# Optimization experiments

Hardware: AMD Instinct MI355X
Metric: run time of the kernel (lower is better)

The kernel has to match this reference:

```python
import jax, jax.numpy as jnp
import numpy as np

MEAN = 0.0
SIGMA = 2.0


def setup_inputs() -> dict:
    key = jax.random.key(0)
    B, S, D = 8, 1024, 1024
    ks = jax.random.split(key, 7)
    scale = 1.0 / np.sqrt(D)
    return {
        "x": jax.random.normal(ks[0], (B, S, D), dtype=jnp.float32),
        "Wa": jax.random.normal(ks[1], (D, D), dtype=jnp.float32) * scale,
        "ba": jnp.zeros((D,), dtype=jnp.float32),
        "Wshift": jax.random.normal(ks[2], (D, D), dtype=jnp.float32) * scale,
        "bshift": jnp.zeros((D,), dtype=jnp.float32),
        "Wscale": jax.random.normal(ks[3], (D, D), dtype=jnp.float32) * scale,
        "bscale": jnp.zeros((D,), dtype=jnp.float32),
    }


def _gaussian_matrix(S, dtype):
    # Row t holds the flipped, normalized Gaussian kernel of length t+1:
    # weight on position j (j<=t) is exp(-((t-j)-mean)^2/(2*sigma^2)), row-normalized.
    idx = jnp.arange(S)
    d = idx[:, None] - idx[None, :]  # t - j
    g = jnp.exp(-((d.astype(dtype) - MEAN) ** 2) / (2.0 * SIGMA ** 2))
    g = jnp.where(d >= 0, g, 0.0)  # causal (growing window)
    return g / jnp.sum(g, axis=1, keepdims=True)


def reference(x, Wa, ba, Wshift, bshift, Wscale, bscale):
    S = x.shape[1]
    W = _gaussian_matrix(S, x.dtype)  # [S, S] lower-triangular
    filtered = jnp.einsum("tj,bjd->btd", W, x)  # causal Gaussian-weighted sum
    shift = filtered @ Wshift + bshift
    scale = filtered @ Wscale + bscale
    affine = jax.nn.relu(x @ Wa + ba)
    return scale * affine + shift
```

## Files before the change

### kernel.cpp

```cpp
#include <hip/hip_runtime.h>
#include <stdint.h>

typedef __attribute__((ext_vector_type(8))) __bf16 bf16x8;
typedef __attribute__((ext_vector_type(4))) float f32x4;

__device__ __forceinline__ unsigned short f2bf(float f) {
  union { float f; unsigned int u; } v; v.f = f;
  unsigned int u = v.u;
  u = (u + 0x7FFFu + ((u >> 16) & 1u)) >> 16;
  return (unsigned short)u;
}
__device__ __forceinline__ float bf2f(unsigned int u) {
  union { unsigned int u; float f; } v; v.u = u << 16;
  return v.f;
}

__global__ __launch_bounds__(256) void xconv(
    const float* __restrict__ x, unsigned short* __restrict__ xb)
{
  const size_t i = ((size_t)blockIdx.x * 256 + threadIdx.x) * 8;
  const float4 a = *(const float4*)(x + i);
  const float4 b = *(const float4*)(x + i + 4);
  ushort4 o0, o1;
  o0.x = f2bf(a.x); o0.y = f2bf(a.y); o0.z = f2bf(a.z); o0.w = f2bf(a.w);
  o1.x = f2bf(b.x); o1.y = f2bf(b.y); o1.z = f2bf(b.z); o1.w = f2bf(b.w);
  *(ushort4*)(xb + i) = o0;
  *(ushort4*)(xb + i + 4) = o1;
}

__global__ __launch_bounds__(256) void wconv(
    const float* __restrict__ Wa, const float* __restrict__ Wsh,
    const float* __restrict__ Wsc, unsigned short* __restrict__ Wt3)
{
  const float* W;
  if (blockIdx.z == 0)      W = Wa;
  else if (blockIdx.z == 1) W = Wsh;
  else                      W = Wsc;
  unsigned short* O = Wt3 + (size_t)blockIdx.z * 1024 * 1024;
  const int k0 = blockIdx.x * 64;
  const int n0 = blockIdx.y * 64;
  __shared__ float t[64][65];
  const int r = threadIdx.x >> 4;
  const int c4 = threadIdx.x & 15;
#pragma unroll
  for (int i = 0; i < 4; ++i) {
    const int row = r + i * 16;
    const float4 v = *(const float4*)(W + (size_t)(k0 + row) * 1024 + n0 + c4 * 4);
    t[row][c4 * 4 + 0] = v.x; t[row][c4 * 4 + 1] = v.y;
    t[row][c4 * 4 + 2] = v.z; t[row][c4 * 4 + 3] = v.w;
  }
  __syncthreads();
#pragma unroll
  for (int i = 0; i < 4; ++i) {
    const int nr = r + i * 16;
    ushort4 o;
    o.x = f2bf(t[c4 * 4 + 0][nr]);
    o.y = f2bf(t[c4 * 4 + 1][nr]);
    o.z = f2bf(t[c4 * 4 + 2][nr]);
    o.w = f2bf(t[c4 * 4 + 3][nr]);
    *(ushort4*)(O + (size_t)(n0 + nr) * 1024 + k0 + c4 * 4) = o;
  }
}

__global__ __launch_bounds__(256, 2) void gemm_all(
    const unsigned short* __restrict__ xb, const unsigned short* __restrict__ Wt3,
    const float* __restrict__ ba, const float* __restrict__ bsh,
    const float* __restrict__ bsc, float* __restrict__ out)
{
  __shared__ __attribute__((aligned(16))) char lds[54016];
  unsigned short* sX = (unsigned short*)lds;
  unsigned short* sB = (unsigned short*)(lds + 20480);
  unsigned short* ysh_l = (unsigned short*)lds;
  unsigned short* ysc_l = (unsigned short*)(lds + 18688);
  unsigned short* aff_l = (unsigned short*)(lds + 37376);

  const int tid = threadIdx.x;
  const int lane = tid & 63;
  const int wid = tid >> 6;
  const int wm = wid >> 1;
  const int wn = wid & 1;
  const int lr = lane & 15;
  const int lk = lane >> 4;

  const int bid = blockIdx.x;
  const int xcd = bid & 7;
  const int rr_ = bid >> 3;
  const int ntl = rr_ & 15;
  const int mg  = rr_ >> 4;
  const int bm0 = (xcd + (mg << 3)) * 128;
  const int bn0 = ntl * 64;
  const bool first = (xcd == 0);

  f32x4 acc[3][4][2];
  f32x4 hacc[2][2];
  const f32x4 z = {0.f, 0.f, 0.f, 0.f};
#pragma unroll
  for (int a = 0; a < 3; ++a)
#pragma unroll
    for (int m = 0; m < 4; ++m)
#pragma unroll
      for (int j = 0; j < 2; ++j) acc[a][m][j] = z;
#pragma unroll
  for (int a = 0; a < 2; ++a)
#pragma unroll
    for (int j = 0; j < 2; ++j) hacc[a][j] = z;

  auto stage = [&](int k0) {
#pragma unroll
    for (int p = 0; p < 5; ++p) {
      const int po = (p * 256 + tid) * 16;
      const int row = po >> 7;
      const int lo = po ^ ((row & 7) << 4);
      const int colu = (lo & 127) >> 1;
      int rel = row - 16;
      if (rel < 0 && first) rel = 0;
      if (rel > 127) rel = 0;
      const unsigned short* src = xb + (size_t)(bm0 + rel) * 1024 + k0 + colu;
      __builtin_amdgcn_global_load_lds(
          (const __attribute__((address_space(1))) void*)src,
          (__attribute__((address_space(3))) void*)(sX + (p * 256 + (wid << 6)) * 8),
          16, 0, 0);
    }
#pragma unroll
    for (int mat = 0; mat < 3; ++mat)
#pragma unroll
      for (int p = 0; p < 2; ++p) {
        const int po = (p * 256 + tid) * 16;
        const int row = po >> 7;
        const int lo = po ^ ((row & 7) << 4);
        const int colu = (lo & 127) >> 1;
        const unsigned short* src =
            Wt3 + ((size_t)mat << 20) + (size_t)(bn0 + row) * 1024 + k0 + colu;
        __builtin_amdgcn_global_load_lds(
            (const __attribute__((address_space(1))) void*)src,
            (__attribute__((address_space(3))) void*)(sB + mat * 4096 + (p * 256 + (wid << 6)) * 8),
            16, 0, 0);
      }
  };
  auto rd = [&](const unsigned short* base, int row, int s) -> bf16x8 {
    const int po = row * 128 + (((s * 32 + lk * 8) * 2) ^ ((row & 7) << 4));
    return *(const bf16x8*)((const char*)base + po);
  };

  stage(0);

  for (int kt = 0; kt < 16; ++kt) {
    __syncthreads();

#pragma unroll
    for (int s = 0; s < 2; ++s) {
      bf16x8 ax[4], bb[3][2], hax;
#pragma unroll
      for (int m = 0; m < 4; ++m)
        ax[m] = rd(sX, 16 + wm * 64 + m * 16 + lr, s);
#pragma unroll
      for (int mat = 0; mat < 3; ++mat)
#pragma unroll
        for (int jj = 0; jj < 2; ++jj)
          bb[mat][jj] = rd(sB + mat * 4096, wn * 32 + jj * 16 + lr, s);
      if (wm == 0) hax = rd(sX, lr, s);

      __builtin_amdgcn_s_setprio(1);
#pragma unroll
      for (int m = 0; m < 4; ++m)
#pragma unroll
        for (int mat = 0; mat < 3; ++mat)
#pragma unroll
          for (int jj = 0; jj < 2; ++jj)
            acc[mat][m][jj] = __builtin_amdgcn_mfma_f32_16x16x32_bf16(
                ax[m], bb[mat][jj], acc[mat][m][jj], 0, 0, 0);
      if (wm == 0) {
#pragma unroll
        for (int mat = 1; mat < 3; ++mat)
#pragma unroll
          for (int jj = 0; jj < 2; ++jj)
            hacc[mat - 1][jj] = __builtin_amdgcn_mfma_f32_16x16x32_bf16(
                hax, bb[mat][jj], hacc[mat - 1][jj], 0, 0, 0);
      }
      __builtin_amdgcn_s_setprio(0);
    }

    __syncthreads();
    if (kt + 1 < 16) stage((kt + 1) * 64);
  }

#pragma unroll
  for (int jj = 0; jj < 2; ++jj) {
    const int nn = wn * 32 + jj * 16 + lr;
    const float Ba = ba[bn0 + nn];
#pragma unroll
    for (int m = 0; m < 4; ++m)
#pragma unroll
      for (int q = 0; q < 4; ++q) {
        const int rowL = wm * 64 + m * 16 + lk * 4 + q;
        aff_l[nn * 130 + rowL] = f2bf(fmaxf(acc[0][m][jj][q] + Ba, 0.0f));
        ysh_l[nn * 146 + 15 + rowL] = f2bf(acc[1][m][jj][q]);
        ysc_l[nn * 146 + 15 + rowL] = f2bf(acc[2][m][jj][q]);
      }
    if (wm == 0) {
#pragma unroll
      for (int q = 0; q < 4; ++q) {
        const int hr = lk * 4 + q;
        if (hr > 0) {
          ysh_l[nn * 146 + hr - 1] = f2bf(hacc[0][jj][q]);
          ysc_l[nn * 146 + hr - 1] = f2bf(hacc[1][jj][q]);
        }
      }
    }
  }
  __syncthreads();
  if (first) {
    for (int i = tid; i < 64 * 15; i += 256) {
      const int nn = i / 15, rw = i % 15;
      ysh_l[nn * 146 + rw] = 0;
      ysc_l[nn * 146 + rw] = 0;
    }
  }
  __syncthreads();

  {
    const int nn = tid & 63;
    const int t0 = (tid >> 6) * 32;
    float g[16];
#pragma unroll
    for (int k = 0; k < 16; ++k) g[k] = __expf(-(float)(k * k) * 0.125f);
    float nfull = 0.f;
#pragma unroll
    for (int k = 0; k < 16; ++k) nfull += g[k];
    const float invf = 1.0f / nfull;
    const float bs = bsh[bn0 + nn];
    const float bc = bsc[bn0 + nn];

    float psh[15], psc[15];
#pragma unroll
    for (int i = 0; i < 15; ++i) {
      psh[i] = bf2f(ysh_l[nn * 146 + t0 + i]);
      psc[i] = bf2f(ysc_l[nn * 146 + t0 + i]);
    }

    for (int c = 0; c < 2; ++c) {
      const int T = t0 + c * 16;
      float csh[16], csc[16], av[16];
#pragma unroll
      for (int u = 0; u < 16; ++u) {
        csh[u] = bf2f(ysh_l[nn * 146 + 15 + T + u]);
        csc[u] = bf2f(ysc_l[nn * 146 + 15 + T + u]);
        av[u]  = bf2f(aff_l[nn * 130 + T + u]);
      }
#pragma unroll
      for (int u = 0; u < 16; ++u) {
        float fs = 0.f, fc = 0.f;
#pragma unroll
        for (int k = 0; k < 16; ++k) {
          const int d = u - k;
          const float vs = (d >= 0) ? csh[d] : psh[15 + d];
          const float vc = (d >= 0) ? csc[d] : psc[15 + d];
          fs = fmaf(g[k], vs, fs);
          fc = fmaf(g[k], vc, fc);
        }
        float inv = invf;
        if (first && (T + u) < 15) {
          float sum = 0.f;
#pragma unroll
          for (int k = 0; k < 16; ++k) sum += (k <= T + u) ? g[k] : 0.f;
          inv = 1.0f / sum;
        }
        out[(size_t)(bm0 + T + u) * 1024 + bn0 + nn] =
            (fc * inv + bc) * av[u] + (fs * inv + bs);
      }
#pragma unroll
      for (int i = 0; i < 15; ++i) { psh[i] = csh[i + 1]; psc[i] = csc[i + 1]; }
    }
  }
}

extern "C" void kernel_launch(void* const* d_in, const int* in_sizes, int n_in,
                              void* d_out, int out_size, void* d_ws, size_t ws_size,
                              hipStream_t stream) {
  const float* x   = (const float*)d_in[0];
  const float* Wa  = (const float*)d_in[1];
  const float* ba  = (const float*)d_in[2];
  const float* Wsh = (const float*)d_in[3];
  const float* bsh = (const float*)d_in[4];
  const float* Wsc = (const float*)d_in[5];
  const float* bsc = (const float*)d_in[6];
  float* out = (float*)d_out;

  char* ws = (char*)d_ws;
  unsigned short* xb  = (unsigned short*)(ws);
  unsigned short* Wt3 = (unsigned short*)(ws + (16u << 20));

  hipLaunchKernelGGL(xconv, dim3(4096), dim3(256), 0, stream, x, xb);
  hipLaunchKernelGGL(wconv, dim3(16, 16, 3), dim3(256), 0, stream,
                     Wa, Wsh, Wsc, Wt3);
  hipLaunchKernelGGL(gemm_all, dim3(1024), dim3(256), 0, stream,
                     xb, Wt3, ba, bsh, bsc, out);
}
```

Before: 81.24 us.

## Double-buffer LDS with 256-row M tiles, 512-thread blocks, and merged prep kernel

Merges the x and weight conversion kernels into one launch. The GEMM block now covers 256 rows with 512 threads (8 waves), which halves the 16-row halo recompute overhead per tile. It also double-buffers the X and B tiles in LDS so the next k-slice loads while the current one runs through MFMA, using explicit vmcnt waits and barriers. LDS grows to about 116KB, which may limit occupancy to one block per CU, and the epilogue convolution code now has to be correct for the new tile layout.

Result: faster. 79.39 us (median of 2 runs) (-2.3%).

```diff
diff --git a/kernel.cpp b/kernel.cpp
--- a/kernel.cpp
+++ b/kernel.cpp
@@ -15,31 +15,32 @@
   return v.f;
 }
 
-__global__ __launch_bounds__(256) void xconv(
-    const float* __restrict__ x, unsigned short* __restrict__ xb)
-{
-  const size_t i = ((size_t)blockIdx.x * 256 + threadIdx.x) * 8;
-  const float4 a = *(const float4*)(x + i);
-  const float4 b = *(const float4*)(x + i + 4);
-  ushort4 o0, o1;
-  o0.x = f2bf(a.x); o0.y = f2bf(a.y); o0.z = f2bf(a.z); o0.w = f2bf(a.w);
-  o1.x = f2bf(b.x); o1.y = f2bf(b.y); o1.z = f2bf(b.z); o1.w = f2bf(b.w);
-  *(ushort4*)(xb + i) = o0;
-  *(ushort4*)(xb + i + 4) = o1;
-}
-
-__global__ __launch_bounds__(256) void wconv(
+__global__ __launch_bounds__(256) void prep(
+    const float* __restrict__ x, unsigned short* __restrict__ xb,
     const float* __restrict__ Wa, const float* __restrict__ Wsh,
     const float* __restrict__ Wsc, unsigned short* __restrict__ Wt3)
 {
-  const float* W;
-  if (blockIdx.z == 0)      W = Wa;
-  else if (blockIdx.z == 1) W = Wsh;
-  else                      W = Wsc;
-  unsigned short* O = Wt3 + (size_t)blockIdx.z * 1024 * 1024;
-  const int k0 = blockIdx.x * 64;
-  const int n0 = blockIdx.y * 64;
   __shared__ float t[64][65];
+  int bid = blockIdx.x;
+  if (bid < 4096) {
+    const size_t i = ((size_t)bid * 256 + threadIdx.x) * 8;
+    const float4 a = *(const float4*)(x + i);
+    const float4 b = *(const float4*)(x + i + 4);
+    ushort4 o0, o1;
+    o0.x = f2bf(a.x); o0.y = f2bf(a.y); o0.z = f2bf(a.z); o0.w = f2bf(a.w);
+    o1.x = f2bf(b.x); o1.y = f2bf(b.y); o1.z = f2bf(b.z); o1.w = f2bf(b.w);
+    *(ushort4*)(xb + i) = o0;
+    *(ushort4*)(xb + i + 4) = o1;
+    return;
+  }
+  bid -= 4096;
+  const int z  = bid >> 8;
+  const int yy = (bid >> 4) & 15;
+  const int xx = bid & 15;
+  const float* W = (z == 0) ? Wa : (z == 1) ? Wsh : Wsc;
+  unsigned short* O = Wt3 + ((size_t)z << 20);
+  const int k0 = xx * 64;
+  const int n0 = yy * 64;
   const int r = threadIdx.x >> 4;
   const int c4 = threadIdx.x & 15;
 #pragma unroll
@@ -62,17 +63,19 @@
   }
 }
 
-__global__ __launch_bounds__(256, 2) void gemm_all(
+__global__ __launch_bounds__(512, 2) void gemm_all(
     const unsigned short* __restrict__ xb, const unsigned short* __restrict__ Wt3,
     const float* __restrict__ ba, const float* __restrict__ bsh,
     const float* __restrict__ bsc, float* __restrict__ out)
 {
-  __shared__ __attribute__((aligned(16))) char lds[54016];
-  unsigned short* sX = (unsigned short*)lds;
-  unsigned short* sB = (unsigned short*)(lds + 20480);
-  unsigned short* ysh_l = (unsigned short*)lds;
-  unsigned short* ysc_l = (unsigned short*)(lds + 18688);
-  unsigned short* aff_l = (unsigned short*)(lds + 37376);
+  __shared__ __attribute__((aligned(16))) char lds[118784];
+  unsigned short* const sX0 = (unsigned short*)lds;
+  unsigned short* const sX1 = (unsigned short*)(lds + 34816);
+  unsigned short* const sB0 = (unsigned short*)(lds + 69632);
+  unsigned short* const sB1 = (unsigned short*)(lds + 94208);
+  unsigned short* const ysh_l = (unsigned short*)lds;
+  unsigned short* const ysc_l = (unsigned short*)(lds + 35072);
+  unsigned short* const aff_l = (unsigned short*)(lds + 70144);
 
   const int tid = threadIdx.x;
   const int lane = tid & 63;
@@ -87,9 +90,9 @@
   const int rr_ = bid >> 3;
   const int ntl = rr_ & 15;
   const int mg  = rr_ >> 4;
-  const int bm0 = (xcd + (mg << 3)) * 128;
+  const int bm0 = (xcd + (mg << 3)) * 256;
   const int bn0 = ntl * 64;
-  const bool first = (xcd == 0);
+  const bool first = ((bm0 & 1023) == 0);
 
   f32x4 acc[3][4][2];
   f32x4 hacc[2][2];
@@ -105,60 +108,78 @@
 #pragma unroll
     for (int j = 0; j < 2; ++j) hacc[a][j] = z;
 
-  auto stage = [&](int k0) {
-#pragma unroll
-    for (int p = 0; p < 5; ++p) {
-      const int po = (p * 256 + tid) * 16;
+  auto stage = [&](int k0, unsigned short* dX, unsigned short* dB) {
+#pragma unroll
+    for (int p = 0; p < 4; ++p) {
+      const int po = (p * 512 + tid) * 16;
       const int row = po >> 7;
       const int lo = po ^ ((row & 7) << 4);
       const int colu = (lo & 127) >> 1;
-      int rel = row - 16;
-      if (rel < 0 && first) rel = 0;
-      if (rel > 127) rel = 0;
-      const unsigned short* src = xb + (size_t)(bm0 + rel) * 1024 + k0 + colu;
+      const unsigned short* src = xb + (size_t)(bm0 + row) * 1024 + k0 + colu;
       __builtin_amdgcn_global_load_lds(
           (const __attribute__((address_space(1))) void*)src,
-          (__attribute__((address_space(3))) void*)(sX + (p * 256 + (wid << 6)) * 8),
+          (__attribute__((address_space(3))) void*)(dX + (p * 512 + (wid << 6)) * 8),
           16, 0, 0);
     }
-#pragma unroll
-    for (int mat = 0; mat < 3; ++mat)
-#pragma unroll
-      for (int p = 0; p < 2; ++p) {
-        const int po = (p * 256 + tid) * 16;
-        const int row = po >> 7;
-        const int lo = po ^ ((row & 7) << 4);
-        const int colu = (lo & 127) >> 1;
-        const unsigned short* src =
-            Wt3 + ((size_t)mat << 20) + (size_t)(bn0 + row) * 1024 + k0 + colu;
-        __builtin_amdgcn_global_load_lds(
-            (const __attribute__((address_space(1))) void*)src,
-            (__attribute__((address_space(3))) void*)(sB + mat * 4096 + (p * 256 + (wid << 6)) * 8),
-            16, 0, 0);
-      }
+    if (tid < 128) {
+      const int po = (2048 + tid) * 16;
+      const int row = po >> 7;
+      const int lo = po ^ ((row & 7) << 4);
+      const int colu = (lo & 127) >> 1;
+      int grow = bm0 - 16 + (row - 256);
+      if (first) grow = bm0;
+      const unsigned short* src = xb + (size_t)grow * 1024 + k0 + colu;
+      __builtin_amdgcn_global_load_lds(
+          (const __attribute__((address_space(1))) void*)src,
+          (__attribute__((address_space(3))) void*)(dX + (2048 + (wid << 6)) * 8),
+          16, 0, 0);
+    }
+#pragma unroll
+    for (int mat = 0; mat < 3; ++mat) {
+      const int po = tid * 16;
+      const int row = po >> 7;
+      const int lo = po ^ ((row & 7) << 4);
+      const int colu = (lo & 127) >> 1;
+      const unsigned short* src =
+          Wt3 + ((size_t)mat << 20) + (size_t)(bn0 + row) * 1024 + k0 + colu;
+      __builtin_amdgcn_global_load_lds(
+          (const __attribute__((address_space(1))) void*)src,
+          (__attribute__((address_space(3))) void*)(dB + mat * 4096 + (wid << 6) * 8),
+          16, 0, 0);
+    }
   };
   auto rd = [&](const unsigned short* base, int row, int s) -> bf16x8 {
     const int po = row * 128 + (((s * 32 + lk * 8) * 2) ^ ((row & 7) << 4));
     return *(const bf16x8*)((const char*)base + po);
   };
 
-  stage(0);
+  stage(0, sX0, sB0);
+  unsigned short *sXc = sX0, *sBc = sB0, *sXn = sX1, *sBn = sB1;
 
   for (int kt = 0; kt < 16; ++kt) {
-    __syncthreads();
+    if (kt + 1 < 16) stage((kt + 1) * 64, sXn, sBn);
+
+    if (kt + 1 < 16) {
+      if (wid < 2) asm volatile("s_waitcnt vmcnt(8)" ::: "memory");
+      else         asm volatile("s_waitcnt vmcnt(7)" ::: "memory");
+    } else {
+      asm volatile("s_waitcnt vmcnt(0)" ::: "memory");
+    }
+    __builtin_amdgcn_s_barrier();
+    asm volatile("" ::: "memory");
 
 #pragma unroll
     for (int s = 0; s < 2; ++s) {
       bf16x8 ax[4], bb[3][2], hax;
 #pragma unroll
       for (int m = 0; m < 4; ++m)
-        ax[m] = rd(sX, 16 + wm * 64 + m * 16 + lr, s);
+        ax[m] = rd(sXc, wm * 64 + m * 16 + lr, s);
 #pragma unroll
       for (int mat = 0; mat < 3; ++mat)
 #pragma unroll
         for (int jj = 0; jj < 2; ++jj)
-          bb[mat][jj] = rd(sB + mat * 4096, wn * 32 + jj * 16 + lr, s);
-      if (wm == 0) hax = rd(sX, lr, s);
+          bb[mat][jj] = rd(sBc + mat * 4096, wn * 32 + jj * 16 + lr, s);
+      if (wm == 0) hax = rd(sXc, 256 + lr, s);
 
       __builtin_amdgcn_s_setprio(1);
 #pragma unroll
@@ -180,8 +201,12 @@
       __builtin_amdgcn_s_setprio(0);
     }
 
-    __syncthreads();
-    if (kt + 1 < 16) stage((kt + 1) * 64);
+    asm volatile("s_waitcnt lgkmcnt(0)" ::: "memory");
+    __builtin_amdgcn_s_barrier();
+    asm volatile("" ::: "memory");
+
+    unsigned short* t1 = sXc; sXc = sXn; sXn = t1;
+    unsigned short* t2 = sBc; sBc = sBn; sBn = t2;
   }
 
 #pragma unroll
@@ -193,27 +218,27 @@
 #pragma unroll
       for (int q = 0; q < 4; ++q) {
         const int rowL = wm * 64 + m * 16 + lk * 4 + q;
-        aff_l[nn * 130 + rowL] = f2bf(fmaxf(acc[0][m][jj][q] + Ba, 0.0f));
-        ysh_l[nn * 146 + 15 + rowL] = f2bf(acc[1][m][jj][q]);
-        ysc_l[nn * 146 + 15 + rowL] = f2bf(acc[2][m][jj][q]);
+        aff_l[nn * 258 + rowL] = f2bf(fmaxf(acc[0][m][jj][q] + Ba, 0.0f));
+        ysh_l[nn * 274 + 15 + rowL] = f2bf(acc[1][m][jj][q]);
+        ysc_l[nn * 274 + 15 + rowL] = f2bf(acc[2][m][jj][q]);
       }
     if (wm == 0) {
 #pragma unroll
       for (int q = 0; q < 4; ++q) {
         const int hr = lk * 4 + q;
         if (hr > 0) {
-          ysh_l[nn * 146 + hr - 1] = f2bf(hacc[0][jj][q]);
-          ysc_l[nn * 146 + hr - 1] = f2bf(hacc[1][jj][q]);
+          ysh_l[nn * 274 + hr - 1] = f2bf(hacc[0][jj][q]);
+          ysc_l[nn * 274 + hr - 1] = f2bf(hacc[1][jj][q]);
         }
       }
     }
   }
   __syncthreads();
   if (first) {
-    for (int i = tid; i < 64 * 15; i += 256) {
+    for (int i = tid; i < 64 * 15; i += 512) {
       const int nn = i / 15, rw = i % 15;
-      ysh_l[nn * 146 + rw] = 0;
-      ysc_l[nn * 146 + rw] = 0;
+      ysh_l[nn * 274 + rw] = 0;
+      ysc_l[nn * 274 + rw] = 0;
     }
   }
   __syncthreads();
@@ -234,8 +259,8 @@
     float psh[15], psc[15];
 #pragma unroll
     for (int i = 0; i < 15; ++i) {
-      psh[i] = bf2f(ysh_l[nn * 146 + t0 + i]);
-      psc[i] = bf2f(ysc_l[nn * 146 + t0 + i]);
+      psh[i] = bf2f(ysh_l[nn * 274 + t0 + i]);
+      psc[i] = bf2f(ysc_l[nn * 274 + t0 + i]);
     }
 
     for (int c = 0; c < 2; ++c) {
@@ -243,9 +268,9 @@
       float csh[16], csc[16], av[16];
 #pragma unroll
       for (int u = 0; u < 16; ++u) {
-        csh[u] = bf2f(ysh_l[nn * 146 + 15 + T + u]);
-        csc[u] = bf2f(ysc_l[nn * 146 + 15 + T + u]);
-        av[u]  = bf2f(aff_l[nn * 130 + T + u]);
+        csh[u] = bf2f(ysh_l[nn * 274 + 15 + T + u]);
+        csc[u] = bf2f(ysc_l[nn * 274 + 15 + T + u]);
+        av[u]  = bf2f(aff_l[nn * 258 + T + u]);
       }
 #pragma unroll
       for (int u = 0; u < 16; ++u) {
@@ -290,9 +315,8 @@
   unsigned short* xb  = (unsigned short*)(ws);
   unsigned short* Wt3 = (unsigned short*)(ws + (16u << 20));
 
-  hipLaunchKernelGGL(xconv, dim3(4096), dim3(256), 0, stream, x, xb);
-  hipLaunchKernelGGL(wconv, dim3(16, 16, 3), dim3(256), 0, stream,
-                     Wa, Wsh, Wsc, Wt3);
-  hipLaunchKernelGGL(gemm_all, dim3(1024), dim3(256), 0, stream,
+  hipLaunchKernelGGL(prep, dim3(4096 + 768), dim3(256), 0, stream,
+                     x, xb, Wa, Wsh, Wsc, Wt3);
+  hipLaunchKernelGGL(gemm_all, dim3(512), dim3(512), 0, stream,
                      xb, Wt3, ba, bsh, bsc, out);
 }
```

## Merge conversion kernels, move halo rows to end of LDS tile, raise occupancy

Applied to the files above, without the earlier changes.

Fuses the x and weight bf16 conversion kernels into one launch to save a kernel launch and let both run concurrently. In the GEMM, the 16-row halo used for the Gaussian-filter history now sits after the 128 main rows in LDS and is loaded by half the threads, and the B tile offset is shifted to match. Launch bounds are raised from 2 to 3 blocks per CU to increase occupancy, at the risk of register pressure or spills given the large accumulator set. The LDS footprint stays at about 54 KB, so three resident blocks may not actually fit.

Result: slower. 125.6 us (+54.6%).

```diff
diff --git a/kernel.cpp b/kernel.cpp
--- a/kernel.cpp
+++ b/kernel.cpp
@@ -15,31 +15,32 @@
   return v.f;
 }
 
-__global__ __launch_bounds__(256) void xconv(
-    const float* __restrict__ x, unsigned short* __restrict__ xb)
-{
-  const size_t i = ((size_t)blockIdx.x * 256 + threadIdx.x) * 8;
-  const float4 a = *(const float4*)(x + i);
-  const float4 b = *(const float4*)(x + i + 4);
-  ushort4 o0, o1;
-  o0.x = f2bf(a.x); o0.y = f2bf(a.y); o0.z = f2bf(a.z); o0.w = f2bf(a.w);
-  o1.x = f2bf(b.x); o1.y = f2bf(b.y); o1.z = f2bf(b.z); o1.w = f2bf(b.w);
-  *(ushort4*)(xb + i) = o0;
-  *(ushort4*)(xb + i + 4) = o1;
-}
-
-__global__ __launch_bounds__(256) void wconv(
+__global__ __launch_bounds__(256) void prep(
+    const float* __restrict__ x, unsigned short* __restrict__ xb,
     const float* __restrict__ Wa, const float* __restrict__ Wsh,
     const float* __restrict__ Wsc, unsigned short* __restrict__ Wt3)
 {
-  const float* W;
-  if (blockIdx.z == 0)      W = Wa;
-  else if (blockIdx.z == 1) W = Wsh;
-  else                      W = Wsc;
-  unsigned short* O = Wt3 + (size_t)blockIdx.z * 1024 * 1024;
-  const int k0 = blockIdx.x * 64;
-  const int n0 = blockIdx.y * 64;
   __shared__ float t[64][65];
+  int bid = blockIdx.x;
+  if (bid < 4096) {
+    const size_t i = ((size_t)bid * 256 + threadIdx.x) * 8;
+    const float4 a = *(const float4*)(x + i);
+    const float4 b = *(const float4*)(x + i + 4);
+    ushort4 o0, o1;
+    o0.x = f2bf(a.x); o0.y = f2bf(a.y); o0.z = f2bf(a.z); o0.w = f2bf(a.w);
+    o1.x = f2bf(b.x); o1.y = f2bf(b.y); o1.z = f2bf(b.z); o1.w = f2bf(b.w);
+    *(ushort4*)(xb + i) = o0;
+    *(ushort4*)(xb + i + 4) = o1;
+    return;
+  }
+  bid -= 4096;
+  const int z  = bid >> 8;
+  const int yy = (bid >> 4) & 15;
+  const int xx = bid & 15;
+  const float* W = (z == 0) ? Wa : (z == 1) ? Wsh : Wsc;
+  unsigned short* O = Wt3 + ((size_t)z << 20);
+  const int k0 = xx * 64;
+  const int n0 = yy * 64;
   const int r = threadIdx.x >> 4;
   const int c4 = threadIdx.x & 15;
 #pragma unroll
@@ -62,17 +63,17 @@
   }
 }
 
-__global__ __launch_bounds__(256, 2) void gemm_all(
+__global__ __launch_bounds__(256, 3) void gemm_all(
     const unsigned short* __restrict__ xb, const unsigned short* __restrict__ Wt3,
     const float* __restrict__ ba, const float* __restrict__ bsh,
     const float* __restrict__ bsc, float* __restrict__ out)
 {
   __shared__ __attribute__((aligned(16))) char lds[54016];
-  unsigned short* sX = (unsigned short*)lds;
-  unsigned short* sB = (unsigned short*)(lds + 20480);
-  unsigned short* ysh_l = (unsigned short*)lds;
-  unsigned short* ysc_l = (unsigned short*)(lds + 18688);
-  unsigned short* aff_l = (unsigned short*)(lds + 37376);
+  unsigned short* const sX = (unsigned short*)lds;
+  unsigned short* const sB = (unsigned short*)(lds + 18432);
+  unsigned short* const ysh_l = (unsigned short*)lds;
+  unsigned short* const ysc_l = (unsigned short*)(lds + 18688);
+  unsigned short* const aff_l = (unsigned short*)(lds + 37376);
 
   const int tid = threadIdx.x;
   const int lane = tid & 63;
@@ -89,7 +90,7 @@
   const int mg  = rr_ >> 4;
   const int bm0 = (xcd + (mg << 3)) * 128;
   const int bn0 = ntl * 64;
-  const bool first = (xcd == 0);
+  const bool first = ((bm0 & 1023) == 0);
 
   f32x4 acc[3][4][2];
   f32x4 hacc[2][2];
@@ -107,18 +108,28 @@
 
   auto stage = [&](int k0) {
 #pragma unroll
-    for (int p = 0; p < 5; ++p) {
+    for (int p = 0; p < 4; ++p) {
       const int po = (p * 256 + tid) * 16;
       const int row = po >> 7;
       const int lo = po ^ ((row & 7) << 4);
       const int colu = (lo & 127) >> 1;
-      int rel = row - 16;
-      if (rel < 0 && first) rel = 0;
-      if (rel > 127) rel = 0;
-      const unsigned short* src = xb + (size_t)(bm0 + rel) * 1024 + k0 + colu;
+      const unsigned short* src = xb + (size_t)(bm0 + row) * 1024 + k0 + colu;
       __builtin_amdgcn_global_load_lds(
           (const __attribute__((address_space(1))) void*)src,
           (__attribute__((address_space(3))) void*)(sX + (p * 256 + (wid << 6)) * 8),
+          16, 0, 0);
+    }
+    if (tid < 128) {
+      const int po = 16384 + tid * 16;
+      const int row = po >> 7;
+      const int lo = po ^ ((row & 7) << 4);
+      const int colu = (lo & 127) >> 1;
+      int grow = bm0 - 16 + (row - 128);
+      if (first) grow = bm0;
+      const unsigned short* src = xb + (size_t)grow * 1024 + k0 + colu;
+      __builtin_amdgcn_global_load_lds(
+          (const __attribute__((address_space(1))) void*)src,
+          (__attribute__((address_space(3))) void*)(sX + 8192 + (wid << 6) * 8),
           16, 0, 0);
     }
 #pragma unroll
@@ -152,13 +163,13 @@
       bf16x8 ax[4], bb[3][2], hax;
 #pragma unroll
       for (int m = 0; m < 4; ++m)
-        ax[m] = rd(sX, 16 + wm * 64 + m * 16 + lr, s);
+        ax[m] = rd(sX, wm * 64 + m * 16 + lr, s);
 #pragma unroll
       for (int mat = 0; mat < 3; ++mat)
 #pragma unroll
         for (int jj = 0; jj < 2; ++jj)
           bb[mat][jj] = rd(sB + mat * 4096, wn * 32 + jj * 16 + lr, s);
-      if (wm == 0) hax = rd(sX, lr, s);
+      if (wm == 0) hax = rd(sX, 128 + lr, s);
 
       __builtin_amdgcn_s_setprio(1);
 #pragma unroll
@@ -290,9 +301,8 @@
   unsigned short* xb  = (unsigned short*)(ws);
   unsigned short* Wt3 = (unsigned short*)(ws + (16u << 20));
 
-  hipLaunchKernelGGL(xconv, dim3(4096), dim3(256), 0, stream, x, xb);
-  hipLaunchKernelGGL(wconv, dim3(16, 16, 3), dim3(256), 0, stream,
-                     Wa, Wsh, Wsc, Wt3);
+  hipLaunchKernelGGL(prep, dim3(4096 + 768), dim3(256), 0, stream,
+                     x, xb, Wa, Wsh, Wsc, Wt3);
   hipLaunchKernelGGL(gemm_all, dim3(1024), dim3(256), 0, stream,
                      xb, Wt3, ba, bsh, bsc, out);
 }
```
